# Kernel optimization log

Hardware: AMD Instinct MI355X
Metric: run time of the kernel (lower is better)

The kernel has to match this reference:

```python
import jax, jax.numpy as jnp
import numpy as np
import math

B, S, D, H, V = 2, 2048, 512, 4, 32000
WINDOWS = [None, 128, 512, None]  # per-head attention windows (None = unlimited)


def setup_inputs() -> dict:
    key = jax.random.key(0)
    ks = jax.random.split(key, 8)
    input_ids = jax.random.randint(ks[0], (B, S), 0, V, dtype=jnp.int64)
    padding_mask = jnp.zeros((B, S), dtype=bool)  # True = pad
    embed_table = jax.random.normal(ks[1], (V, D), dtype=jnp.float32) * 0.02
    self_factors = jnp.full((H,), 0.1, dtype=jnp.float32)
    distance_alphas = jnp.full((H,), 0.1, dtype=jnp.float32)
    # torch Linear weights: [out_features, in_features], xavier-uniform init
    lim_f = math.sqrt(6.0 / (H * D + D))
    fusion_w = jax.random.uniform(ks[2], (D, H * D), jnp.float32, -lim_f, lim_f)
    fusion_b = jnp.zeros((D,), jnp.float32)
    lim_o = math.sqrt(6.0 / (D + V))
    out_w = jax.random.uniform(ks[3], (V, D), jnp.float32, -lim_o, lim_o)
    out_b = jnp.zeros((V,), jnp.float32)
    return {
        "input_ids": input_ids,
        "padding_mask": padding_mask,
        "embed_table": embed_table,
        "self_factors": self_factors,
        "distance_alphas": distance_alphas,
        "fusion_w": fusion_w,
        "fusion_b": fusion_b,
        "out_w": out_w,
        "out_b": out_b,
    }


def reference(input_ids, padding_mask, embed_table, self_factors,
              distance_alphas, fusion_w, fusion_b, out_w, out_b):
    b, s = input_ids.shape
    d = embed_table.shape[1]
    h = self_factors.shape[0]

    emb = embed_table[input_ids]  # [B,S,D]

    pos = jnp.arange(s)
    dist = jnp.abs(pos[:, None] - pos[None, :])          # [S,S]
    causal = pos[None, :] > pos[:, None]                  # [S,S] strict upper triangle
    eye = dist == 0                                       # [S,S]

    # shared raw scores, computed once (same for all heads)
    base = jnp.einsum('bqd,bkd->bqk', emb, emb) / math.sqrt(d)  # [B,S,S]

    # per-head distance decay bias: [H,S,S]
    decay = 1.0 / (1.0 + distance_alphas[:, None, None] * dist.astype(jnp.float32))

    scores = base[None, :, :, :] * decay[:, None, :, :]   # [H,B,S,S]
    # diagonal self-factor scaling
    scores = jnp.where(eye[None, None],
                       scores * self_factors[:, None, None, None], scores)

    # per-head window mask (None -> window >= S, never masks)
    win = jnp.array([s if w is None else w for w in WINDOWS[:h]])
    window_mask = dist[None, :, :] > win[:, None, None]   # [H,S,S]

    # key padding mask, diagonal exempted (as in original)
    key_pad = padding_mask[:, None, :] & (~eye[None])      # [B,S,S]

    full_mask = (window_mask[:, None] | causal[None, None] | key_pad[None])  # [H,B,S,S]
    scores = jnp.where(full_mask, -jnp.inf, scores)

    attn = jax.nn.softmax(scores, axis=-1)                 # [H,B,S,S]
    ctx = jnp.einsum('hbqk,bkd->hbqd', attn, emb)          # [H,B,S,D]

    concat = jnp.moveaxis(ctx, 0, 2).reshape(b, s, h * d)  # [B,S,H*D]
    fused = concat @ fusion_w.T + fusion_b                 # [B,S,D]
    logits = fused @ out_w.T + out_b                       # [B,S,V]
    return logits
```

## Files before the change

kernel.cpp:

```cpp
#include <hip/hip_runtime.h>
#include <hip/hip_bf16.h>
#include <stdint.h>

#define BB 2
#define SB 2048
#define DD 512
#define HH 4
#define VV 32000

typedef __attribute__((ext_vector_type(4))) float f32x4;
typedef __attribute__((ext_vector_type(8))) short bf16x8;
typedef __attribute__((ext_vector_type(4))) unsigned short us4;

__device__ __forceinline__ unsigned short f2bf(float f) {
    unsigned u = __float_as_uint(f);
    u += 0x7fffu + ((u >> 16) & 1u);
    return (unsigned short)(u >> 16);
}

__device__ __forceinline__ __attribute__((address_space(3))) unsigned int*
as_lds(void* p) {
    return (__attribute__((address_space(3))) unsigned int*)(unsigned)(uintptr_t)p;
}
__device__ __forceinline__ const __attribute__((address_space(1))) unsigned int*
as_gbl(const void* p) {
    return (const __attribute__((address_space(1))) unsigned int*)(uintptr_t)p;
}

__device__ __forceinline__ bf16x8 ldsrd(const unsigned short* base, int row, int g) {
    int byte = row * 64 + (((g) ^ (row & 3)) << 4);
    return *(const bf16x8*)((const char*)base + byte);
}

__global__ void k_prep(const int* __restrict__ ids, const float* __restrict__ tbl,
                       const float* __restrict__ als,
                       const float* __restrict__ fw, const float* __restrict__ ow,
                       unsigned short* __restrict__ outw_bf, unsigned short* __restrict__ fusw_bf,
                       unsigned short* __restrict__ emb, unsigned short* __restrict__ embT,
                       float* __restrict__ dtab, float* __restrict__ lsum)
{
    __shared__ unsigned short TT[64][72];
    const int bid = blockIdx.x, t = threadIdx.x;

    if (bid < 2000) {
        int base = bid * 8192 + t * 4;
#pragma unroll
        for (int it = 0; it < 8; ++it) {
            int i = base + it * 1024;
            float4 v = *(const float4*)(ow + i);
            us4 o; o.x = f2bf(v.x); o.y = f2bf(v.y); o.z = f2bf(v.z); o.w = f2bf(v.w);
            *(us4*)(outw_bf + i) = o;
        }
    } else if (bid < 2256) {
        int base = (bid - 2000) * 4096 + t * 4;
#pragma unroll
        for (int it = 0; it < 4; ++it) {
            int i = base + it * 1024;
            float4 v = *(const float4*)(fw + i);
            us4 o; o.x = f2bf(v.x); o.y = f2bf(v.y); o.z = f2bf(v.z); o.w = f2bf(v.w);
            *(us4*)(fusw_bf + i) = o;
        }
    } else if (bid < 6352) {
        int row = bid - 2256;
        int id = ids[row];
        if (id < 0) id = 0;
        if (id >= VV) id = VV - 1;
        const float* s = tbl + (size_t)id * DD;
        unsigned short* d = emb + (size_t)row * DD;
        d[t]       = f2bf(s[t]);
        d[t + 256] = f2bf(s[t + 256]);
    } else if (bid < 6448) {
        int i = (bid - 6352) * 256 + t;
        if (i < HH * SB) {
            int h = i >> 11, dd = i & (SB - 1);
            dtab[i] = 0.04419417382415922f / (1.f + als[h] * (float)dd);
        } else {
            lsum[i - HH * SB] = 0.f;
        }
    } else {
        int bid2 = bid - 6448;
        const int d0 = (bid2 & 7) * 64, s0 = ((bid2 >> 3) & 31) * 64, b = bid2 >> 8;
        {
            int s = t >> 2, c16 = (t & 3) * 16;
            int id = ids[b * SB + s0 + s];
            if (id < 0) id = 0;
            if (id >= VV) id = VV - 1;
            const float* src = tbl + (size_t)id * DD + d0 + c16;
#pragma unroll
            for (int q4 = 0; q4 < 4; ++q4) {
                float4 v = *(const float4*)(src + q4 * 4);
                TT[c16 + q4 * 4 + 0][s] = f2bf(v.x);
                TT[c16 + q4 * 4 + 1][s] = f2bf(v.y);
                TT[c16 + q4 * 4 + 2][s] = f2bf(v.z);
                TT[c16 + q4 * 4 + 3][s] = f2bf(v.w);
            }
        }
        __syncthreads();
        {
            int d = t >> 2, sc = (t & 3) * 16;
            bf16x8 o0, o1;
#pragma unroll
            for (int j = 0; j < 8; ++j) {
                o0[j] = (short)TT[d][sc + j];
                o1[j] = (short)TT[d][sc + 8 + j];
            }
            unsigned short* dst = embT + ((size_t)(b * DD + d0 + d)) * SB + s0 + sc;
            *(bf16x8*)dst = o0;
            *(bf16x8*)(dst + 8) = o1;
        }
    }
}

__launch_bounds__(256, 2)
__global__ void k_base(const unsigned short* __restrict__ emb,
                       const unsigned char* __restrict__ pad,
                       const float* __restrict__ sfs,
                       const float* __restrict__ dtab,
                       unsigned short* __restrict__ P,
                       float* __restrict__ lsum)
{
    const int kt = blockIdx.x, qt = blockIdx.y, b = blockIdx.z;
    if (kt > qt + 1) return;
    const int tid = threadIdx.x, lane = tid & 63, wv = tid >> 6;
    const int l15 = lane & 15, g = lane >> 4;

    if (kt == qt + 1) {
        int row = tid >> 2, cb = (tid & 3) * 16;
        int4 z = {0, 0, 0, 0};
#pragma unroll
        for (int h = 0; h < 4; ++h) {
            unsigned short* Ph = P + (((size_t)(h * 2 + b)) * SB + qt * 64 + row) * SB + kt * 64 + cb;
            *(int4*)Ph = z;
            *(int4*)(Ph + 8) = z;
        }
        return;
    }

    __shared__ __align__(16) unsigned short Ql[64 * 128];
    __shared__ __align__(16) unsigned short Kl[64 * 128];

    const int q = qt * 64 + wv * 16 + l15;

    f32x4 zero4 = {0.f, 0.f, 0.f, 0.f};
    f32x4 cc[4];
#pragma unroll
    for (int c = 0; c < 4; ++c) cc[c] = zero4;

    for (int dc = 0; dc < 4; ++dc) {
        const int d0 = dc * 128;
        __syncthreads();
#pragma unroll
        for (int i = 0; i < 4; ++i) {
            int flat = (i * 256 + tid) * 8;
            int row = flat >> 7;
            int ch  = (flat >> 3) & 15;
            int scol = ((ch ^ (row & 15)) << 3);
            __builtin_amdgcn_global_load_lds(
                as_gbl(emb + ((size_t)(b * SB + qt * 64 + row)) * DD + d0 + scol),
                as_lds(Ql + flat), 16, 0, 0);
            __builtin_amdgcn_global_load_lds(
                as_gbl(emb + ((size_t)(b * SB + kt * 64 + row)) * DD + d0 + scol),
                as_lds(Kl + flat), 16, 0, 0);
        }
        asm volatile("s_waitcnt vmcnt(0)" ::: "memory");
        __syncthreads();

#pragma unroll
        for (int dsl = 0; dsl < 4; ++dsl) {
            int chr = (dsl * 4 + g);
            bf16x8 qf = *(const bf16x8*)(Ql + (wv * 16 + l15) * 128 + ((chr ^ l15) << 3));
#pragma unroll
            for (int c = 0; c < 4; ++c) {
                bf16x8 kf = *(const bf16x8*)(Kl + (c * 16 + l15) * 128 + ((chr ^ l15) << 3));
                cc[c] = __builtin_amdgcn_mfma_f32_16x16x32_bf16(kf, qf, cc[c], 0, 0, 0);
            }
        }
    }

    unsigned long long padm = __ballot(pad[(size_t)b * SB + kt * 64 + lane] != 0);

    const int wins[4] = {1 << 30, 128, 512, 1 << 30};
#pragma unroll
    for (int h = 0; h < 4; ++h) {
        const int win = wins[h];
        if (kt * 64 + win + 192 < qt * 64) continue;
        const float sf = sfs[h];
        const float* dth = dtab + h * SB;
        float rsum = 0.f;
        unsigned short pb[4][4];
#pragma unroll
        for (int c = 0; c < 4; ++c) {
#pragma unroll
            for (int r = 0; r < 4; ++r) {
                int kk = kt * 64 + c * 16 + 4 * g + r;
                int dist = q - kk;
                float p = 0.f;
                if (dist >= 0 && dist <= win &&
                    ((dist == 0) || !((padm >> (c * 16 + 4 * g + r)) & 1ull))) {
                    float s = cc[c][r] * dth[dist];
                    if (dist == 0) s *= sf;
                    p = __expf(s);
                }
                rsum += p;
                pb[c][r] = f2bf(p);
            }
        }
        unsigned short* Ph = P + (((size_t)(h * 2 + b)) * SB + q) * SB + kt * 64;
#pragma unroll
        for (int c = 0; c < 4; ++c) {
            us4 o;
            o.x = pb[c][0]; o.y = pb[c][1]; o.z = pb[c][2]; o.w = pb[c][3];
            *(us4*)(Ph + c * 16 + 4 * g) = o;
        }
        rsum += __shfl_xor(rsum, 16, 64);
        rsum += __shfl_xor(rsum, 32, 64);
        if (lane < 16)
            atomicAdd(&lsum[((size_t)(h * 2 + b)) * SB + q], rsum);
    }
}

__launch_bounds__(256, 2)
__global__ void k_pv(const unsigned short* __restrict__ P,
                     const unsigned short* __restrict__ embT,
                     const float* __restrict__ lsum,
                     unsigned short* __restrict__ concat)
{
    const int t64 = blockIdx.x, b = blockIdx.y, h = blockIdx.z;
    const int mt = t64 >> 2, nt = t64 & 3;
    const int Q0 = mt * 128;
    const int win = (h == 1) ? 128 : (h == 2) ? 512 : (1 << 30);
    int klo = Q0 - win - 64; if (klo < 0) klo = 0; klo &= ~63;
    const int khi = Q0 + 128;

    __shared__ __align__(16) unsigned short Al[128 * 32];
    __shared__ __align__(16) unsigned short Bl[128 * 32];

    const int tid = threadIdx.x, lane = tid & 63, wv = tid >> 6;
    const int wm = (wv >> 1) * 64, wn = (wv & 1) * 64;
    const int l15 = lane & 15, g = lane >> 4;

    f32x4 zero4 = {0.f, 0.f, 0.f, 0.f};
    f32x4 acc[4][4];
#pragma unroll
    for (int i = 0; i < 4; ++i)
#pragma unroll
        for (int j = 0; j < 4; ++j) acc[i][j] = zero4;

    const unsigned short* Ab = P + (((size_t)(h * 2 + b)) * SB + Q0) * SB;
    const unsigned short* Bb = embT + ((size_t)(b * DD + nt * 128)) * SB;

    for (int k0 = klo; k0 < khi; k0 += 32) {
        __syncthreads();
#pragma unroll
        for (int s = 0; s < 2; ++s) {
            int e = (s * 256 + tid) * 8;
            int row = e >> 5, col = e & 31;
            __builtin_amdgcn_global_load_lds(as_gbl(Ab + (size_t)row * SB + k0 + col),
                                             as_lds(Al + e), 16, 0, 0);
            __builtin_amdgcn_global_load_lds(as_gbl(Bb + (size_t)row * SB + k0 + col),
                                             as_lds(Bl + e), 16, 0, 0);
        }
        asm volatile("s_waitcnt vmcnt(0)" ::: "memory");
        __syncthreads();

        bf16x8 af[4], bfr[4];
#pragma unroll
        for (int i = 0; i < 4; ++i) {
            af[i]  = *(const bf16x8*)(Al + (wm + i * 16 + l15) * 32 + 8 * g);
            bfr[i] = *(const bf16x8*)(Bl + (wn + i * 16 + l15) * 32 + 8 * g);
        }
#pragma unroll
        for (int i = 0; i < 4; ++i)
#pragma unroll
            for (int j = 0; j < 4; ++j)
                acc[i][j] = __builtin_amdgcn_mfma_f32_16x16x32_bf16(af[i], bfr[j], acc[i][j], 0, 0, 0);
    }

    const float* ls = lsum + ((size_t)(h * 2 + b)) * SB;
    unsigned short* cb = concat + ((size_t)(b * SB)) * (HH * DD) + h * DD + nt * 128;
#pragma unroll
    for (int i = 0; i < 4; ++i) {
        int rowb = wm + i * 16 + g * 4;
        float inv[4];
#pragma unroll
        for (int rr = 0; rr < 4; ++rr) inv[rr] = 1.f / ls[Q0 + rowb + rr];
#pragma unroll
        for (int j = 0; j < 4; ++j) {
            int col = wn + j * 16 + l15;
#pragma unroll
            for (int rr = 0; rr < 4; ++rr)
                cb[(size_t)(Q0 + rowb + rr) * (HH * DD) + col] = f2bf(acc[i][j][rr] * inv[rr]);
        }
    }
}

template <int OUTF32>
__launch_bounds__(256, 2)
__global__ void k_gemm_bt(const unsigned short* __restrict__ A,
                          const unsigned short* __restrict__ Bt,
                          const float* __restrict__ bias,
                          void* __restrict__ Cout,
                          int M, int N, int K)
{
    const int nMt = M >> 7;
    const int nwg = gridDim.x;
    int bid = blockIdx.x;
    int q = nwg >> 3, r = nwg & 7;
    int x = bid & 7, o = bid >> 3;
    int wg = (x < r ? x * (q + 1) : r * (q + 1) + (x - r) * q) + o;
    const int mt = wg % nMt, nt = wg / nMt;

    __shared__ __align__(16) unsigned short Al[128 * 32];
    __shared__ __align__(16) unsigned short Bl[128 * 32];

    const int tid = threadIdx.x;
    const int lane = tid & 63;
    const int wv = tid >> 6;
    const int wm = (wv >> 1) * 64, wn = (wv & 1) * 64;
    const int l15 = lane & 15, g = lane >> 4;

    f32x4 zero4 = {0.f, 0.f, 0.f, 0.f};
    f32x4 acc[4][4];
#pragma unroll
    for (int i = 0; i < 4; ++i)
#pragma unroll
        for (int j = 0; j < 4; ++j) acc[i][j] = zero4;

    const unsigned short* Ab = A + (size_t)mt * 128 * K;
    const unsigned short* Bb = Bt + (size_t)nt * 128 * K;

    for (int k0 = 0; k0 < K; k0 += 32) {
        __syncthreads();
#pragma unroll
        for (int s = 0; s < 2; ++s) {
            int e = (s * 256 + tid) * 8;
            int row = e >> 5, col = e & 31;
            __builtin_amdgcn_global_load_lds(as_gbl(Ab + (size_t)row * K + k0 + col),
                                             as_lds(Al + e), 16, 0, 0);
            __builtin_amdgcn_global_load_lds(as_gbl(Bb + (size_t)row * K + k0 + col),
                                             as_lds(Bl + e), 16, 0, 0);
        }
        asm volatile("s_waitcnt vmcnt(0)" ::: "memory");
        __syncthreads();

        bf16x8 af[4], bfr[4];
#pragma unroll
        for (int i = 0; i < 4; ++i) {
            af[i]  = *(const bf16x8*)(Al + (wm + i * 16 + l15) * 32 + 8 * g);
            bfr[i] = *(const bf16x8*)(Bl + (wn + i * 16 + l15) * 32 + 8 * g);
        }
#pragma unroll
        for (int i = 0; i < 4; ++i)
#pragma unroll
            for (int j = 0; j < 4; ++j)
                acc[i][j] = __builtin_amdgcn_mfma_f32_16x16x32_bf16(af[i], bfr[j], acc[i][j], 0, 0, 0);
    }

#pragma unroll
    for (int i = 0; i < 4; ++i) {
        int rowb = mt * 128 + wm + i * 16 + g * 4;
#pragma unroll
        for (int j = 0; j < 4; ++j) {
            int col = nt * 128 + wn + j * 16 + l15;
            float bv = bias[col];
            if (OUTF32) {
                float* C = (float*)Cout;
#pragma unroll
                for (int rr = 0; rr < 4; ++rr)
                    C[(size_t)(rowb + rr) * N + col] = acc[i][j][rr] + bv;
            } else {
                unsigned short* C = (unsigned short*)Cout;
#pragma unroll
                for (int rr = 0; rr < 4; ++rr)
                    C[(size_t)(rowb + rr) * N + col] = f2bf(acc[i][j][rr] + bv);
            }
        }
    }
}

__launch_bounds__(512, 2)
__global__ void k_gemm256(const unsigned short* __restrict__ A,
                          const unsigned short* __restrict__ Bt,
                          const float* __restrict__ bias,
                          float* __restrict__ Cout,
                          int M, int N, int K)
{
    const int nMt = M >> 8;
    const int nwg = gridDim.x;
    int bid = blockIdx.x;
    int q = nwg >> 3, r = nwg & 7;
    int x = bid & 7, o = bid >> 3;
    int wg = (x < r ? x * (q + 1) : r * (q + 1) + (x - r) * q) + o;
    const int mt = wg % nMt, nt = wg / nMt;

    __shared__ __align__(16) unsigned short Al[4][8192];
    __shared__ __align__(16) unsigned short Bl[4][8192];

    const int tid = threadIdx.x;
    const int lane = tid & 63, wv = tid >> 6;
    const int wr = wv >> 2, wc = wv & 3;
    const int l15 = lane & 15, g = lane >> 4;

    f32x4 zero4 = {0.f, 0.f, 0.f, 0.f};
    f32x4 acc[8][4];
#pragma unroll
    for (int i = 0; i < 8; ++i)
#pragma unroll
        for (int j = 0; j < 4; ++j) acc[i][j] = zero4;

    const unsigned short* Ab = A + (size_t)mt * 256 * K;
    const unsigned short* Bb = Bt + (size_t)nt * 256 * K;

    const int c0 = tid, c1 = 512 + tid;
    const int r0 = c0 >> 2, r1 = c1 >> 2;
    const int sc0 = (((c0 & 3) ^ (r0 & 3)) << 3);
    const int sc1 = (((c1 & 3) ^ (r1 & 3)) << 3);
    const unsigned short* Asrc0 = Ab + (size_t)r0 * K + sc0;
    const unsigned short* Asrc1 = Ab + (size_t)r1 * K + sc1;
    const unsigned short* Bsrc0 = Bb + (size_t)r0 * K + sc0;
    const unsigned short* Bsrc1 = Bb + (size_t)r1 * K + sc1;

#define STAGE_A256(rg_, ko_) { \
    __builtin_amdgcn_global_load_lds(as_gbl(Asrc0 + (ko_)), as_lds(&Al[rg_][c0 * 8]), 16, 0, 0); \
    __builtin_amdgcn_global_load_lds(as_gbl(Asrc1 + (ko_)), as_lds(&Al[rg_][c1 * 8]), 16, 0, 0); }
#define STAGE_B256(rg_, ko_) { \
    __builtin_amdgcn_global_load_lds(as_gbl(Bsrc0 + (ko_)), as_lds(&Bl[rg_][c0 * 8]), 16, 0, 0); \
    __builtin_amdgcn_global_load_lds(as_gbl(Bsrc1 + (ko_)), as_lds(&Bl[rg_][c1 * 8]), 16, 0, 0); }

#define SBAR { __builtin_amdgcn_sched_barrier(0); __builtin_amdgcn_s_barrier(); __builtin_amdgcn_sched_barrier(0); }

#define GEMM_GROUP(t_, DOSTAGE_, WAIT_)                                          \
  {                                                                              \
    const int rg = (t_) & 3;                                                     \
    const unsigned short* Ar = Al[rg];                                           \
    const unsigned short* Br = Bl[rg];                                           \
    bf16x8 bfr0 = ldsrd(Br, wc * 64 +  0 + l15, g);                              \
    bf16x8 bfr1 = ldsrd(Br, wc * 64 + 16 + l15, g);                              \
    bf16x8 bfr2 = ldsrd(Br, wc * 64 + 32 + l15, g);                              \
    bf16x8 bfr3 = ldsrd(Br, wc * 64 + 48 + l15, g);                              \
    bf16x8 af0 = ldsrd(Ar, wr * 128 +  0 + l15, g);                              \
    bf16x8 af1 = ldsrd(Ar, wr * 128 + 16 + l15, g);                              \
    bf16x8 af2 = ldsrd(Ar, wr * 128 + 32 + l15, g);                              \
    bf16x8 af3 = ldsrd(Ar, wr * 128 + 48 + l15, g);                              \
    if (DOSTAGE_) STAGE_A256(((t_) + 3) & 3, ((t_) + 3) * 32);                   \
    SBAR;                                                                        \
    __builtin_amdgcn_s_setprio(1);                                               \
    acc[0][0] = __builtin_amdgcn_mfma_f32_16x16x32_bf16(af0, bfr0, acc[0][0], 0, 0, 0); \
    acc[0][1] = __builtin_amdgcn_mfma_f32_16x16x32_bf16(af0, bfr1, acc[0][1], 0, 0, 0); \
    acc[0][2] = __builtin_amdgcn_mfma_f32_16x16x32_bf16(af0, bfr2, acc[0][2], 0, 0, 0); \
    acc[0][3] = __builtin_amdgcn_mfma_f32_16x16x32_bf16(af0, bfr3, acc[0][3], 0, 0, 0); \
    acc[1][0] = __builtin_amdgcn_mfma_f32_16x16x32_bf16(af1, bfr0, acc[1][0], 0, 0, 0); \
    acc[1][1] = __builtin_amdgcn_mfma_f32_16x16x32_bf16(af1, bfr1, acc[1][1], 0, 0, 0); \
    acc[1][2] = __builtin_amdgcn_mfma_f32_16x16x32_bf16(af1, bfr2, acc[1][2], 0, 0, 0); \
    acc[1][3] = __builtin_amdgcn_mfma_f32_16x16x32_bf16(af1, bfr3, acc[1][3], 0, 0, 0); \
    acc[2][0] = __builtin_amdgcn_mfma_f32_16x16x32_bf16(af2, bfr0, acc[2][0], 0, 0, 0); \
    acc[2][1] = __builtin_amdgcn_mfma_f32_16x16x32_bf16(af2, bfr1, acc[2][1], 0, 0, 0); \
    acc[2][2] = __builtin_amdgcn_mfma_f32_16x16x32_bf16(af2, bfr2, acc[2][2], 0, 0, 0); \
    acc[2][3] = __builtin_amdgcn_mfma_f32_16x16x32_bf16(af2, bfr3, acc[2][3], 0, 0, 0); \
    acc[3][0] = __builtin_amdgcn_mfma_f32_16x16x32_bf16(af3, bfr0, acc[3][0], 0, 0, 0); \
    acc[3][1] = __builtin_amdgcn_mfma_f32_16x16x32_bf16(af3, bfr1, acc[3][1], 0, 0, 0); \
    acc[3][2] = __builtin_amdgcn_mfma_f32_16x16x32_bf16(af3, bfr2, acc[3][2], 0, 0, 0); \
    acc[3][3] = __builtin_amdgcn_mfma_f32_16x16x32_bf16(af3, bfr3, acc[3][3], 0, 0, 0); \
    __builtin_amdgcn_s_setprio(0);                                               \
    SBAR;                                                                        \
    bf16x8 ag0 = ldsrd(Ar, wr * 128 +  64 + l15, g);                             \
    bf16x8 ag1 = ldsrd(Ar, wr * 128 +  80 + l15, g);                             \
    bf16x8 ag2 = ldsrd(Ar, wr * 128 +  96 + l15, g);                             \
    bf16x8 ag3 = ldsrd(Ar, wr * 128 + 112 + l15, g);                             \
    if (DOSTAGE_) STAGE_B256(((t_) + 3) & 3, ((t_) + 3) * 32);                   \
    WAIT_;                                                                       \
    SBAR;                                                                        \
    __builtin_amdgcn_s_setprio(1);                                               \
    acc[4][0] = __builtin_amdgcn_mfma_f32_16x16x32_bf16(ag0, bfr0, acc[4][0], 0, 0, 0); \
    acc[4][1] = __builtin_amdgcn_mfma_f32_16x16x32_bf16(ag0, bfr1, acc[4][1], 0, 0, 0); \
    acc[4][2] = __builtin_amdgcn_mfma_f32_16x16x32_bf16(ag0, bfr2, acc[4][2], 0, 0, 0); \
    acc[4][3] = __builtin_amdgcn_mfma_f32_16x16x32_bf16(ag0, bfr3, acc[4][3], 0, 0, 0); \
    acc[5][0] = __builtin_amdgcn_mfma_f32_16x16x32_bf16(ag1, bfr0, acc[5][0], 0, 0, 0); \
    acc[5][1] = __builtin_amdgcn_mfma_f32_16x16x32_bf16(ag1, bfr1, acc[5][1], 0, 0, 0); \
    acc[5][2] = __builtin_amdgcn_mfma_f32_16x16x32_bf16(ag1, bfr2, acc[5][2], 0, 0, 0); \
    acc[5][3] = __builtin_amdgcn_mfma_f32_16x16x32_bf16(ag1, bfr3, acc[5][3], 0, 0, 0); \
    acc[6][0] = __builtin_amdgcn_mfma_f32_16x16x32_bf16(ag2, bfr0, acc[6][0], 0, 0, 0); \
    acc[6][1] = __builtin_amdgcn_mfma_f32_16x16x32_bf16(ag2, bfr1, acc[6][1], 0, 0, 0); \
    acc[6][2] = __builtin_amdgcn_mfma_f32_16x16x32_bf16(ag2, bfr2, acc[6][2], 0, 0, 0); \
    acc[6][3] = __builtin_amdgcn_mfma_f32_16x16x32_bf16(ag2, bfr3, acc[6][3], 0, 0, 0); \
    acc[7][0] = __builtin_amdgcn_mfma_f32_16x16x32_bf16(ag3, bfr0, acc[7][0], 0, 0, 0); \
    acc[7][1] = __builtin_amdgcn_mfma_f32_16x16x32_bf16(ag3, bfr1, acc[7][1], 0, 0, 0); \
    acc[7][2] = __builtin_amdgcn_mfma_f32_16x16x32_bf16(ag3, bfr2, acc[7][2], 0, 0, 0); \
    acc[7][3] = __builtin_amdgcn_mfma_f32_16x16x32_bf16(ag3, bfr3, acc[7][3], 0, 0, 0); \
    __builtin_amdgcn_s_setprio(0);                                               \
    SBAR;                                                                        \
  }

    const int NT = K >> 5;
    STAGE_A256(0, 0);  STAGE_B256(0, 0);
    STAGE_A256(1, 32); STAGE_B256(1, 32);
    STAGE_A256(2, 64); STAGE_B256(2, 64);
    asm volatile("s_waitcnt vmcnt(8)" ::: "memory");
    SBAR;

    for (int t = 0; t < NT - 3; ++t) {
        GEMM_GROUP(t, 1, asm volatile("s_waitcnt vmcnt(8)" ::: "memory"));
    }
    GEMM_GROUP(NT - 3, 0, asm volatile("s_waitcnt vmcnt(4)" ::: "memory"));
    GEMM_GROUP(NT - 2, 0, asm volatile("s_waitcnt vmcnt(0)" ::: "memory"));
    GEMM_GROUP(NT - 1, 0, );

    const int mrow = mt * 256 + wr * 128;
    const int ncol = nt * 256 + wc * 64;
#pragma unroll
    for (int i = 0; i < 8; ++i) {
        int rowb = mrow + i * 16 + g * 4;
#pragma unroll
        for (int j = 0; j < 4; ++j) {
            int col = ncol + j * 16 + l15;
            float bv = bias[col];
#pragma unroll
            for (int rr = 0; rr < 4; ++rr)
                Cout[(size_t)(rowb + rr) * N + col] = acc[i][j][rr] + bv;
        }
    }
#undef GEMM_GROUP
#undef STAGE_A256
#undef STAGE_B256
#undef SBAR
}

extern "C" void kernel_launch(void* const* d_in, const int* in_sizes, int n_in,
                              void* d_out, int out_size, void* d_ws, size_t ws_size,
                              hipStream_t stream)
{
    const int*           ids = (const int*)d_in[0];
    const unsigned char* pad = (const unsigned char*)d_in[1];
    const float*         tbl = (const float*)d_in[2];
    const float*         sfs = (const float*)d_in[3];
    const float*         als = (const float*)d_in[4];
    const float*         fw  = (const float*)d_in[5];
    const float*         fb  = (const float*)d_in[6];
    const float*         ow  = (const float*)d_in[7];
    const float*         ob  = (const float*)d_in[8];
    float* logits = (float*)d_out;

    char* ws = (char*)d_ws;
    unsigned short* outw_bf = (unsigned short*)(ws);
    unsigned short* fusw_bf = (unsigned short*)(ws + 32768000);
    unsigned short* emb_bf  = (unsigned short*)(ws + 34865152);
    unsigned short* concat  = (unsigned short*)(ws + 39059456);
    unsigned short* fused   = (unsigned short*)(ws + 55836672);

    char* ob_scratch = (char*)d_out;
    unsigned short* P    = (unsigned short*)(ob_scratch);
    unsigned short* embT = (unsigned short*)(ob_scratch + 67108864);
    float*          dtab = (float*)(ob_scratch + 71303168);
    float*          lsum = (float*)(ob_scratch + 71335936);

    k_prep<<<6960, 256, 0, stream>>>(ids, tbl, als, fw, ow,
                                     outw_bf, fusw_bf, emb_bf, embT, dtab, lsum);

    dim3 bg(32, 32, BB);
    k_base<<<bg, 256, 0, stream>>>(emb_bf, pad, sfs, dtab, P, lsum);

    dim3 pg(64, BB, HH);
    k_pv<<<pg, 256, 0, stream>>>(P, embT, lsum, concat);

    k_gemm_bt<0><<<32 * 4, 256, 0, stream>>>(concat, fusw_bf, fb, fused, BB * SB, DD, HH * DD);
    k_gemm256<<<16 * 125, 512, 0, stream>>>(fused, outw_bf, ob, logits, BB * SB, VV, DD);
}
```

Measured before the change: 386.5 us.

## Rewrite logits GEMM with K=64 double-buffered tiles and simpler sync

The output-projection GEMM switches from a 4-stage ring of K=32 tiles with hand-placed waitcnts and split A/B staging to a 2-stage double buffer of K=64 tiles. Each iteration prefetches the next tile and runs two K=32 sub-steps of 32 MFMAs, then synchronises with __syncthreads, which cuts the barrier count per K. The LDS swizzle widens to 8 chunks per 128-byte row, and launch bounds drop to 1 block per CU because LDS use grows. The cost is fewer resident waves and a coarser pipeline that may expose global-load latency.

```diff
diff --git a/kernel.cpp b/kernel.cpp
--- a/kernel.cpp
+++ b/kernel.cpp
@@ -27,9 +27,8 @@
     return (const __attribute__((address_space(1))) unsigned int*)(uintptr_t)p;
 }
 
-__device__ __forceinline__ bf16x8 ldsrd(const unsigned short* base, int row, int g) {
-    int byte = row * 64 + (((g) ^ (row & 3)) << 4);
-    return *(const bf16x8*)((const char*)base + byte);
+__device__ __forceinline__ bf16x8 ldsrd64(const unsigned short* base, int row, int c) {
+    return *(const bf16x8*)((const char*)base + row * 128 + ((c ^ (row & 7)) << 4));
 }
 
 __global__ void k_prep(const int* __restrict__ ids, const float* __restrict__ tbl,
@@ -378,12 +377,12 @@
     }
 }
 
-__launch_bounds__(512, 2)
-__global__ void k_gemm256(const unsigned short* __restrict__ A,
-                          const unsigned short* __restrict__ Bt,
-                          const float* __restrict__ bias,
-                          float* __restrict__ Cout,
-                          int M, int N, int K)
+__launch_bounds__(512, 1)
+__global__ void k_logits(const unsigned short* __restrict__ A,
+                         const unsigned short* __restrict__ Bt,
+                         const float* __restrict__ bias,
+                         float* __restrict__ Cout,
+                         int M, int N, int K)
 {
     const int nMt = M >> 8;
     const int nwg = gridDim.x;
@@ -393,11 +392,10 @@
     int wg = (x < r ? x * (q + 1) : r * (q + 1) + (x - r) * q) + o;
     const int mt = wg % nMt, nt = wg / nMt;
 
-    __shared__ __align__(16) unsigned short Al[4][8192];
-    __shared__ __align__(16) unsigned short Bl[4][8192];
-
-    const int tid = threadIdx.x;
-    const int lane = tid & 63, wv = tid >> 6;
+    __shared__ __align__(16) unsigned short Al[2][256 * 64];
+    __shared__ __align__(16) unsigned short Bl[2][256 * 64];
+
+    const int tid = threadIdx.x, lane = tid & 63, wv = tid >> 6;
     const int wr = wv >> 2, wc = wv & 3;
     const int l15 = lane & 15, g = lane >> 4;
 
@@ -411,99 +409,57 @@
     const unsigned short* Ab = A + (size_t)mt * 256 * K;
     const unsigned short* Bb = Bt + (size_t)nt * 256 * K;
 
-    const int c0 = tid, c1 = 512 + tid;
-    const int r0 = c0 >> 2, r1 = c1 >> 2;
-    const int sc0 = (((c0 & 3) ^ (r0 & 3)) << 3);
-    const int sc1 = (((c1 & 3) ^ (r1 & 3)) << 3);
-    const unsigned short* Asrc0 = Ab + (size_t)r0 * K + sc0;
-    const unsigned short* Asrc1 = Ab + (size_t)r1 * K + sc1;
-    const unsigned short* Bsrc0 = Bb + (size_t)r0 * K + sc0;
-    const unsigned short* Bsrc1 = Bb + (size_t)r1 * K + sc1;
-
-#define STAGE_A256(rg_, ko_) { \
-    __builtin_amdgcn_global_load_lds(as_gbl(Asrc0 + (ko_)), as_lds(&Al[rg_][c0 * 8]), 16, 0, 0); \
-    __builtin_amdgcn_global_load_lds(as_gbl(Asrc1 + (ko_)), as_lds(&Al[rg_][c1 * 8]), 16, 0, 0); }
-#define STAGE_B256(rg_, ko_) { \
-    __builtin_amdgcn_global_load_lds(as_gbl(Bsrc0 + (ko_)), as_lds(&Bl[rg_][c0 * 8]), 16, 0, 0); \
-    __builtin_amdgcn_global_load_lds(as_gbl(Bsrc1 + (ko_)), as_lds(&Bl[rg_][c1 * 8]), 16, 0, 0); }
-
-#define SBAR { __builtin_amdgcn_sched_barrier(0); __builtin_amdgcn_s_barrier(); __builtin_amdgcn_sched_barrier(0); }
-
-#define GEMM_GROUP(t_, DOSTAGE_, WAIT_)                                          \
-  {                                                                              \
-    const int rg = (t_) & 3;                                                     \
-    const unsigned short* Ar = Al[rg];                                           \
-    const unsigned short* Br = Bl[rg];                                           \
-    bf16x8 bfr0 = ldsrd(Br, wc * 64 +  0 + l15, g);                              \
-    bf16x8 bfr1 = ldsrd(Br, wc * 64 + 16 + l15, g);                              \
-    bf16x8 bfr2 = ldsrd(Br, wc * 64 + 32 + l15, g);                              \
-    bf16x8 bfr3 = ldsrd(Br, wc * 64 + 48 + l15, g);                              \
-    bf16x8 af0 = ldsrd(Ar, wr * 128 +  0 + l15, g);                              \
-    bf16x8 af1 = ldsrd(Ar, wr * 128 + 16 + l15, g);                              \
-    bf16x8 af2 = ldsrd(Ar, wr * 128 + 32 + l15, g);                              \
-    bf16x8 af3 = ldsrd(Ar, wr * 128 + 48 + l15, g);                              \
-    if (DOSTAGE_) STAGE_A256(((t_) + 3) & 3, ((t_) + 3) * 32);                   \
-    SBAR;                                                                        \
-    __builtin_amdgcn_s_setprio(1);                                               \
-    acc[0][0] = __builtin_amdgcn_mfma_f32_16x16x32_bf16(af0, bfr0, acc[0][0], 0, 0, 0); \
-    acc[0][1] = __builtin_amdgcn_mfma_f32_16x16x32_bf16(af0, bfr1, acc[0][1], 0, 0, 0); \
-    acc[0][2] = __builtin_amdgcn_mfma_f32_16x16x32_bf16(af0, bfr2, acc[0][2], 0, 0, 0); \
-    acc[0][3] = __builtin_amdgcn_mfma_f32_16x16x32_bf16(af0, bfr3, acc[0][3], 0, 0, 0); \
-    acc[1][0] = __builtin_amdgcn_mfma_f32_16x16x32_bf16(af1, bfr0, acc[1][0], 0, 0, 0); \
-    acc[1][1] = __builtin_amdgcn_mfma_f32_16x16x32_bf16(af1, bfr1, acc[1][1], 0, 0, 0); \
-    acc[1][2] = __builtin_amdgcn_mfma_f32_16x16x32_bf16(af1, bfr2, acc[1][2], 0, 0, 0); \
-    acc[1][3] = __builtin_amdgcn_mfma_f32_16x16x32_bf16(af1, bfr3, acc[1][3], 0, 0, 0); \
-    acc[2][0] = __builtin_amdgcn_mfma_f32_16x16x32_bf16(af2, bfr0, acc[2][0], 0, 0, 0); \
-    acc[2][1] = __builtin_amdgcn_mfma_f32_16x16x32_bf16(af2, bfr1, acc[2][1], 0, 0, 0); \
-    acc[2][2] = __builtin_amdgcn_mfma_f32_16x16x32_bf16(af2, bfr2, acc[2][2], 0, 0, 0); \
-    acc[2][3] = __builtin_amdgcn_mfma_f32_16x16x32_bf16(af2, bfr3, acc[2][3], 0, 0, 0); \
-    acc[3][0] = __builtin_amdgcn_mfma_f32_16x16x32_bf16(af3, bfr0, acc[3][0], 0, 0, 0); \
-    acc[3][1] = __builtin_amdgcn_mfma_f32_16x16x32_bf16(af3, bfr1, acc[3][1], 0, 0, 0); \
-    acc[3][2] = __builtin_amdgcn_mfma_f32_16x16x32_bf16(af3, bfr2, acc[3][2], 0, 0, 0); \
-    acc[3][3] = __builtin_amdgcn_mfma_f32_16x16x32_bf16(af3, bfr3, acc[3][3], 0, 0, 0); \
-    __builtin_amdgcn_s_setprio(0);                                               \
-    SBAR;                                                                        \
-    bf16x8 ag0 = ldsrd(Ar, wr * 128 +  64 + l15, g);                             \
-    bf16x8 ag1 = ldsrd(Ar, wr * 128 +  80 + l15, g);                             \
-    bf16x8 ag2 = ldsrd(Ar, wr * 128 +  96 + l15, g);                             \
-    bf16x8 ag3 = ldsrd(Ar, wr * 128 + 112 + l15, g);                             \
-    if (DOSTAGE_) STAGE_B256(((t_) + 3) & 3, ((t_) + 3) * 32);                   \
-    WAIT_;                                                                       \
-    SBAR;                                                                        \
-    __builtin_amdgcn_s_setprio(1);                                               \
-    acc[4][0] = __builtin_amdgcn_mfma_f32_16x16x32_bf16(ag0, bfr0, acc[4][0], 0, 0, 0); \
-    acc[4][1] = __builtin_amdgcn_mfma_f32_16x16x32_bf16(ag0, bfr1, acc[4][1], 0, 0, 0); \
-    acc[4][2] = __builtin_amdgcn_mfma_f32_16x16x32_bf16(ag0, bfr2, acc[4][2], 0, 0, 0); \
-    acc[4][3] = __builtin_amdgcn_mfma_f32_16x16x32_bf16(ag0, bfr3, acc[4][3], 0, 0, 0); \
-    acc[5][0] = __builtin_amdgcn_mfma_f32_16x16x32_bf16(ag1, bfr0, acc[5][0], 0, 0, 0); \
-    acc[5][1] = __builtin_amdgcn_mfma_f32_16x16x32_bf16(ag1, bfr1, acc[5][1], 0, 0, 0); \
-    acc[5][2] = __builtin_amdgcn_mfma_f32_16x16x32_bf16(ag1, bfr2, acc[5][2], 0, 0, 0); \
-    acc[5][3] = __builtin_amdgcn_mfma_f32_16x16x32_bf16(ag1, bfr3, acc[5][3], 0, 0, 0); \
-    acc[6][0] = __builtin_amdgcn_mfma_f32_16x16x32_bf16(ag2, bfr0, acc[6][0], 0, 0, 0); \
-    acc[6][1] = __builtin_amdgcn_mfma_f32_16x16x32_bf16(ag2, bfr1, acc[6][1], 0, 0, 0); \
-    acc[6][2] = __builtin_amdgcn_mfma_f32_16x16x32_bf16(ag2, bfr2, acc[6][2], 0, 0, 0); \
-    acc[6][3] = __builtin_amdgcn_mfma_f32_16x16x32_bf16(ag2, bfr3, acc[6][3], 0, 0, 0); \
-    acc[7][0] = __builtin_amdgcn_mfma_f32_16x16x32_bf16(ag3, bfr0, acc[7][0], 0, 0, 0); \
-    acc[7][1] = __builtin_amdgcn_mfma_f32_16x16x32_bf16(ag3, bfr1, acc[7][1], 0, 0, 0); \
-    acc[7][2] = __builtin_amdgcn_mfma_f32_16x16x32_bf16(ag3, bfr2, acc[7][2], 0, 0, 0); \
-    acc[7][3] = __builtin_amdgcn_mfma_f32_16x16x32_bf16(ag3, bfr3, acc[7][3], 0, 0, 0); \
-    __builtin_amdgcn_s_setprio(0);                                               \
-    SBAR;                                                                        \
-  }
-
-    const int NT = K >> 5;
-    STAGE_A256(0, 0);  STAGE_B256(0, 0);
-    STAGE_A256(1, 32); STAGE_B256(1, 32);
-    STAGE_A256(2, 64); STAGE_B256(2, 64);
-    asm volatile("s_waitcnt vmcnt(8)" ::: "memory");
-    SBAR;
-
-    for (int t = 0; t < NT - 3; ++t) {
-        GEMM_GROUP(t, 1, asm volatile("s_waitcnt vmcnt(8)" ::: "memory"));
-    }
-    GEMM_GROUP(NT - 3, 0, asm volatile("s_waitcnt vmcnt(4)" ::: "memory"));
-    GEMM_GROUP(NT - 2, 0, asm volatile("s_waitcnt vmcnt(0)" ::: "memory"));
-    GEMM_GROUP(NT - 1, 0, );
+    const unsigned short* As[4];
+    const unsigned short* Bs[4];
+    int ldst[4];
+#pragma unroll
+    for (int j = 0; j < 4; ++j) {
+        int ch = tid + j * 512;
+        int row = ch >> 3, cpos = ch & 7;
+        int scol = ((cpos ^ (row & 7)) << 3);
+        As[j] = Ab + (size_t)row * K + scol;
+        Bs[j] = Bb + (size_t)row * K + scol;
+        ldst[j] = ch * 8;
+    }
+
+#define STG(bufi_, k0_) {                                                         \
+    _Pragma("unroll")                                                             \
+    for (int j = 0; j < 4; ++j)                                                   \
+        __builtin_amdgcn_global_load_lds(as_gbl(As[j] + (k0_)),                   \
+                                         as_lds(&Al[bufi_][ldst[j]]), 16, 0, 0);  \
+    _Pragma("unroll")                                                             \
+    for (int j = 0; j < 4; ++j)                                                   \
+        __builtin_amdgcn_global_load_lds(as_gbl(Bs[j] + (k0_)),                   \
+                                         as_lds(&Bl[bufi_][ldst[j]]), 16, 0, 0); }
+
+    STG(0, 0);
+    __syncthreads();
+
+    for (int t = 0; t < 8; ++t) {
+        const int cur = t & 1;
+        if (t < 7) STG(cur ^ 1, (t + 1) * 64);
+        const unsigned short* Ar = Al[cur];
+        const unsigned short* Br = Bl[cur];
+#pragma unroll
+        for (int s = 0; s < 2; ++s) {
+            bf16x8 bf[4], af[8];
+#pragma unroll
+            for (int n = 0; n < 4; ++n)
+                bf[n] = ldsrd64(Br, wc * 64 + n * 16 + l15, s * 4 + g);
+#pragma unroll
+            for (int m = 0; m < 8; ++m)
+                af[m] = ldsrd64(Ar, wr * 128 + m * 16 + l15, s * 4 + g);
+            __builtin_amdgcn_s_setprio(1);
+#pragma unroll
+            for (int m = 0; m < 8; ++m)
+#pragma unroll
+                for (int n = 0; n < 4; ++n)
+                    acc[m][n] = __builtin_amdgcn_mfma_f32_16x16x32_bf16(af[m], bf[n], acc[m][n], 0, 0, 0);
+            __builtin_amdgcn_s_setprio(0);
+        }
+        __syncthreads();
+    }
+#undef STG
 
     const int mrow = mt * 256 + wr * 128;
     const int ncol = nt * 256 + wc * 64;
@@ -519,10 +475,6 @@
                 Cout[(size_t)(rowb + rr) * N + col] = acc[i][j][rr] + bv;
         }
     }
-#undef GEMM_GROUP
-#undef STAGE_A256
-#undef STAGE_B256
-#undef SBAR
 }
 
 extern "C" void kernel_launch(void* const* d_in, const int* in_sizes, int n_in,
@@ -563,5 +515,5 @@
     k_pv<<<pg, 256, 0, stream>>>(P, embT, lsum, concat);
 
     k_gemm_bt<0><<<32 * 4, 256, 0, stream>>>(concat, fusw_bf, fb, fused, BB * SB, DD, HH * DD);
-    k_gemm256<<<16 * 125, 512, 0, stream>>>(fused, outw_bf, ob, logits, BB * SB, VV, DD);
-}
+    k_logits<<<16 * 125, 512, 0, stream>>>(fused, outw_bf, ob, logits, BB * SB, VV, DD);
+}
```

Measured after the change: 379.6 us. Within noise of the previous version (-1.8%).
